# Kernel optimization log

Measured on AMD Instinct MI355X. Metric: run time of the kernel, lower is better.

The kernel has to match this reference:

```python
import jax, jax.numpy as jnp
import numpy as np

NUM_NODES = 1_000_000
MEM_DIM = 100
TIME_DIM = 100
EDGE_DIM = 172
HIDDEN = 128  # TGN_DECODER_HIDDEN
E = 500_000
IN_DIM = MEM_DIM * 2 + TIME_DIM + EDGE_DIM  # 472


def setup_inputs() -> dict:
    key = jax.random.key(0)
    ks = jax.random.split(key, 12)
    src = jax.random.randint(ks[0], (E,), 0, NUM_NODES)
    dst = jax.random.randint(ks[1], (E,), 0, NUM_NODES)
    t = jax.random.uniform(ks[2], (E,), dtype=jnp.float32) * 1000.0
    edge_attr = jax.random.normal(ks[3], (E, EDGE_DIM), dtype=jnp.float32)
    memory = jax.random.normal(ks[4], (NUM_NODES, MEM_DIM), dtype=jnp.float32)
    last_update = jax.random.uniform(ks[5], (NUM_NODES,), dtype=jnp.float32) * 500.0
    # TimeEncoder: cos(Linear(1, time_dim))
    time_w = jax.random.normal(ks[6], (TIME_DIM,), dtype=jnp.float32) / jnp.sqrt(1.0)
    time_b = jax.random.normal(ks[7], (TIME_DIM,), dtype=jnp.float32)
    # growth head: Linear(IN_DIM, HIDDEN) -> ReLU -> Linear(HIDDEN, 1)
    w1 = jax.random.normal(ks[8], (IN_DIM, HIDDEN), dtype=jnp.float32) / jnp.sqrt(IN_DIM)
    b1 = jnp.zeros((HIDDEN,), dtype=jnp.float32)
    w2 = jax.random.normal(ks[9], (HIDDEN, 1), dtype=jnp.float32) / jnp.sqrt(HIDDEN)
    b2 = jnp.zeros((1,), dtype=jnp.float32)
    return {"src": src, "dst": dst, "t": t, "edge_attr": edge_attr,
            "memory": memory, "last_update": last_update,
            "time_w": time_w, "time_b": time_b,
            "w1": w1, "b1": b1, "w2": w2, "b2": b2}


def reference(src, dst, t, edge_attr, memory, last_update, time_w, time_b, w1, b1, w2, b2):
    # Gather per-node memory rows (irregular indexing)
    src_mem = memory[src]                     # [E, MEM_DIM]
    dst_mem = memory[dst]                     # [E, MEM_DIM]
    delta_t = t - last_update[src]            # [E]
    # TimeEncoder: cos(delta_t * w + b)
    dt_enc = jnp.cos(delta_t[:, None] * time_w[None, :] + time_b[None, :])  # [E, TIME_DIM]
    out = jnp.concatenate([src_mem, dst_mem, dt_enc, edge_attr], axis=1)   # [E, IN_DIM]
    h = jax.nn.relu(out @ w1 + b1)            # [E, HIDDEN]
    growth_score = h @ w2 + b2                # [E, 1]
    return growth_score
```

## Files before the change

kernel.cpp:

```cpp
#include <hip/hip_runtime.h>
#include <hip/hip_bf16.h>
#include <math.h>

#define MEM_DIM  100
#define TIME_DIM 100
#define EDGE_DIM 172
#define HIDDEN   128
#define IN_DIM   472
#define K_PAD    480
#define NCHUNK   15
#define BM       256
#define THREADS  1024
#define W1_ELEMS (NCHUNK * 8 * 64 * 8)
#define W1_BYTES (W1_ELEMS * 2)

typedef __attribute__((ext_vector_type(8))) short bf16x8;
typedef __attribute__((ext_vector_type(4))) float floatx4;

typedef const __attribute__((address_space(1))) unsigned int* gp_t;
typedef __attribute__((address_space(3))) unsigned int* lp_t;

__global__ void prep_w1(const float* __restrict__ w1, __hip_bfloat16* __restrict__ w1p) {
    int idx = blockIdx.x * 256 + threadIdx.x;
    if (idx >= K_PAD * HIDDEN) return;
    int k = idx >> 7;
    int n = idx & 127;
    float v = (k < IN_DIM) ? w1[k * HIDDEN + n] : 0.0f;
    int c = k >> 5, kl = k & 31, quad = kl >> 3, j = kl & 7;
    int t = n >> 4, r = n & 15;
    int off = ((c * 8 + t) * 64 + quad * 16 + r) * 8 + j;
    w1p[off] = __float2bfloat16(v);
}

__global__ __launch_bounds__(THREADS, 4)
void tgn_mfma(const int* __restrict__ src, const int* __restrict__ dst,
              const float* __restrict__ t, const float* __restrict__ edge_attr,
              const float* __restrict__ memory, const float* __restrict__ last_update,
              const float* __restrict__ time_w, const float* __restrict__ time_b,
              const __hip_bfloat16* __restrict__ w1p, const float* __restrict__ b1,
              const float* __restrict__ w2, const float* __restrict__ b2,
              float* __restrict__ out, int E)
{
    extern __shared__ __hip_bfloat16 W1s[];
    __shared__ int   s_src[BM];
    __shared__ int   s_dst[BM];
    __shared__ float s_dt[BM];
    __shared__ float s_tw[TIME_DIM], s_tb[TIME_DIM];
    __shared__ float s_b1[HIDDEN], s_w2[HIDDEN];
    __shared__ float s_out[BM];

    const int tid  = threadIdx.x;
    const int e0   = blockIdx.x * BM;
    const int g    = tid >> 6;
    const int lane = tid & 63;
    const int quad = (tid >> 4) & 3;
    const int r    = tid & 15;

    #pragma unroll
    for (int i = 0; i < 8; ++i) {
        int off = i * (THREADS * 16) + tid * 16;
        if (off < W1_BYTES) {
            __builtin_amdgcn_global_load_lds(
                (gp_t)(const void*)((const char*)w1p + off),
                (lp_t)(void*)((char*)W1s + off), 16, 0, 0);
        }
    }
    if (tid < BM) {
        int e = e0 + tid; if (e >= E) e = E - 1;
        int s = src[e];
        s_src[tid] = s;
        s_dst[tid] = dst[e];
        s_dt[tid]  = t[e] - last_update[s];
    }
    if (tid < HIDDEN) { s_b1[tid] = b1[tid]; s_w2[tid] = w2[tid]; }
    if (tid < TIME_DIM) { s_tw[tid] = time_w[tid]; s_tb[tid] = time_b[tid]; }
    __syncthreads();

    const int m = g * 16 + r;
    const float* srcrow = memory + (long)s_src[m] * MEM_DIM;
    const float* dstrow = memory + (long)s_dst[m] * MEM_DIM;
    int em = e0 + m; if (em >= E) em = E - 1;
    const float* earow = edge_attr + (long)em * EDGE_DIM;
    const float dt = s_dt[m];

    floatx4 acc[8];
    #pragma unroll
    for (int i = 0; i < 8; ++i) acc[i] = (floatx4){0.f, 0.f, 0.f, 0.f};

    #pragma unroll
    for (int c = 0; c < NCHUNK; ++c) {
        const int kb = c * 32 + quad * 8;
        float v[8];
        if (kb + 7 < MEM_DIM) {
            float4 lo = *(const float4*)(srcrow + kb);
            float4 hi = *(const float4*)(srcrow + kb + 4);
            v[0]=lo.x; v[1]=lo.y; v[2]=lo.z; v[3]=lo.w;
            v[4]=hi.x; v[5]=hi.y; v[6]=hi.z; v[7]=hi.w;
        } else if (kb >= MEM_DIM && kb + 7 < 2 * MEM_DIM) {
            float4 lo = *(const float4*)(dstrow + kb - MEM_DIM);
            float4 hi = *(const float4*)(dstrow + kb - MEM_DIM + 4);
            v[0]=lo.x; v[1]=lo.y; v[2]=lo.z; v[3]=lo.w;
            v[4]=hi.x; v[5]=hi.y; v[6]=hi.z; v[7]=hi.w;
        } else if (kb >= 200 && kb + 7 < 300) {
            int c0 = kb - 200;
            #pragma unroll
            for (int j = 0; j < 8; ++j)
                v[j] = cosf(dt * s_tw[c0 + j] + s_tb[c0 + j]);
        } else if (kb >= 300 && kb + 7 < IN_DIM) {
            float4 lo = *(const float4*)(earow + kb - 300);
            float4 hi = *(const float4*)(earow + kb - 300 + 4);
            v[0]=lo.x; v[1]=lo.y; v[2]=lo.z; v[3]=lo.w;
            v[4]=hi.x; v[5]=hi.y; v[6]=hi.z; v[7]=hi.w;
        } else {
            #pragma unroll
            for (int j = 0; j < 8; ++j) {
                int k = kb + j;
                float x;
                if (k < MEM_DIM)          x = srcrow[k];
                else if (k < 2 * MEM_DIM) x = dstrow[k - MEM_DIM];
                else if (k < 300)         x = cosf(dt * s_tw[k - 200] + s_tb[k - 200]);
                else if (k < IN_DIM)      x = earow[k - 300];
                else                      x = 0.0f;
                v[j] = x;
            }
        }
        bf16x8 af;
        #pragma unroll
        for (int j = 0; j < 8; ++j)
            af[j] = (short)__bfloat16_as_ushort(__float2bfloat16(v[j]));

        #pragma unroll
        for (int tnum = 0; tnum < 8; ++tnum) {
            bf16x8 bfrag = ((bf16x8*)W1s)[(c * 8 + tnum) * 64 + lane];
            acc[tnum] = __builtin_amdgcn_mfma_f32_16x16x32_bf16(af, bfrag, acc[tnum], 0, 0, 0);
        }
    }

    float part[4] = {0.f, 0.f, 0.f, 0.f};
    #pragma unroll
    for (int tnum = 0; tnum < 8; ++tnum) {
        int n = tnum * 16 + r;
        float b1n = s_b1[n];
        float w2n = s_w2[n];
        #pragma unroll
        for (int reg = 0; reg < 4; ++reg) {
            float h = acc[tnum][reg] + b1n;
            h = h > 0.f ? h : 0.f;
            part[reg] += h * w2n;
        }
    }
    const float b2v = b2[0];
    #pragma unroll
    for (int reg = 0; reg < 4; ++reg) {
        float p = part[reg];
        p += __shfl_xor(p, 1, 64);
        p += __shfl_xor(p, 2, 64);
        p += __shfl_xor(p, 4, 64);
        p += __shfl_xor(p, 8, 64);
        if (r == 0) s_out[g * 16 + quad * 4 + reg] = p + b2v;
    }
    __syncthreads();
    if (tid < BM) {
        int e = e0 + tid;
        if (e < E) out[e] = s_out[tid];
    }
}

extern "C" void kernel_launch(void* const* d_in, const int* in_sizes, int n_in,
                              void* d_out, int out_size, void* d_ws, size_t ws_size,
                              hipStream_t stream) {
    const int*   src = (const int*)d_in[0];
    const int*   dst = (const int*)d_in[1];
    const float* t   = (const float*)d_in[2];
    const float* ea  = (const float*)d_in[3];
    const float* mem = (const float*)d_in[4];
    const float* lu  = (const float*)d_in[5];
    const float* tw  = (const float*)d_in[6];
    const float* tb  = (const float*)d_in[7];
    const float* w1  = (const float*)d_in[8];
    const float* b1  = (const float*)d_in[9];
    const float* w2  = (const float*)d_in[10];
    const float* b2  = (const float*)d_in[11];
    float* out = (float*)d_out;
    const int E = in_sizes[0];

    __hip_bfloat16* w1p = (__hip_bfloat16*)d_ws;

    static bool attr_set = false;
    if (!attr_set) {
        (void)hipFuncSetAttribute(reinterpret_cast<const void*>(tgn_mfma),
                                  hipFuncAttributeMaxDynamicSharedMemorySize,
                                  W1_BYTES);
        attr_set = true;
    }

    prep_w1<<<(K_PAD * HIDDEN + 255) / 256, 256, 0, stream>>>(w1, w1p);

    int grid = (E + BM - 1) / BM;
    tgn_mfma<<<grid, THREADS, W1_BYTES, stream>>>(src, dst, t, ea, mem, lu, tw, tb,
                                                  w1p, b1, w2, b2, out, E);
}
```

Measured before the change: 795.4 us.

## Pad each input segment to 128-wide K blocks and hoist all gather loads

Repacks W1 so each of the four input segments (src mem, dst mem, time enc, edge attr) starts at a 32-aligned chunk boundary, padding K from 480 to 576. Every per-lane load then becomes an aligned float4 with no per-element branching. All memory and edge-attr loads are issued early and the time-encoding MFMAs run first, so gather latency overlaps with compute. The cost is three extra MFMA chunks of zero padding, more LDS for W1 (fewer co-resident blocks possible) and higher register pressure from the hoisted loads.

New measurement: 792.2 us. Within noise of the previous version (-0.4%).

```diff
diff --git a/kernel.cpp b/kernel.cpp
--- a/kernel.cpp
+++ b/kernel.cpp
@@ -7,8 +7,8 @@
 #define EDGE_DIM 172
 #define HIDDEN   128
 #define IN_DIM   472
-#define K_PAD    480
-#define NCHUNK   15
+#define K_PAD    576
+#define NCHUNK   18
 #define BM       256
 #define THREADS  1024
 #define W1_ELEMS (NCHUNK * 8 * 64 * 8)
@@ -20,13 +20,20 @@
 typedef const __attribute__((address_space(1))) unsigned int* gp_t;
 typedef __attribute__((address_space(3))) unsigned int* lp_t;
 
+#define LD4(p) (*(const float4*)(p))
+
 __global__ void prep_w1(const float* __restrict__ w1, __hip_bfloat16* __restrict__ w1p) {
     int idx = blockIdx.x * 256 + threadIdx.x;
     if (idx >= K_PAD * HIDDEN) return;
-    int k = idx >> 7;
-    int n = idx & 127;
-    float v = (k < IN_DIM) ? w1[k * HIDDEN + n] : 0.0f;
-    int c = k >> 5, kl = k & 31, quad = kl >> 3, j = kl & 7;
+    int kp = idx >> 7;
+    int n  = idx & 127;
+    int k; bool valid;
+    if (kp < 128)      { k = kp;              valid = kp < 100; }
+    else if (kp < 256) { k = 100 + kp - 128;  valid = (kp - 128) < 100; }
+    else if (kp < 384) { k = 200 + kp - 256;  valid = (kp - 256) < 100; }
+    else               { k = 300 + kp - 384;  valid = (kp - 384) < 172; }
+    float v = valid ? w1[k * HIDDEN + n] : 0.0f;
+    int c = kp >> 5, kl = kp & 31, quad = kl >> 3, j = kl & 7;
     int t = n >> 4, r = n & 15;
     int off = ((c * 8 + t) * 64 + quad * 16 + r) * 8 + j;
     w1p[off] = __float2bfloat16(v);
@@ -57,13 +64,11 @@
     const int r    = tid & 15;
 
     #pragma unroll
-    for (int i = 0; i < 8; ++i) {
+    for (int i = 0; i < 9; ++i) {
         int off = i * (THREADS * 16) + tid * 16;
-        if (off < W1_BYTES) {
-            __builtin_amdgcn_global_load_lds(
-                (gp_t)(const void*)((const char*)w1p + off),
-                (lp_t)(void*)((char*)W1s + off), 16, 0, 0);
-        }
+        __builtin_amdgcn_global_load_lds(
+            (gp_t)(const void*)((const char*)w1p + off),
+            (lp_t)(void*)((char*)W1s + off), 16, 0, 0);
     }
     if (tid < BM) {
         int e = e0 + tid; if (e >= E) e = E - 1;
@@ -82,58 +87,126 @@
     int em = e0 + m; if (em >= E) em = E - 1;
     const float* earow = edge_attr + (long)em * EDGE_DIM;
     const float dt = s_dt[m];
+    const int qo = quad * 8;
 
     floatx4 acc[8];
     #pragma unroll
     for (int i = 0; i < 8; ++i) acc[i] = (floatx4){0.f, 0.f, 0.f, 0.f};
 
-    #pragma unroll
-    for (int c = 0; c < NCHUNK; ++c) {
-        const int kb = c * 32 + quad * 8;
-        float v[8];
-        if (kb + 7 < MEM_DIM) {
-            float4 lo = *(const float4*)(srcrow + kb);
-            float4 hi = *(const float4*)(srcrow + kb + 4);
-            v[0]=lo.x; v[1]=lo.y; v[2]=lo.z; v[3]=lo.w;
-            v[4]=hi.x; v[5]=hi.y; v[6]=hi.z; v[7]=hi.w;
-        } else if (kb >= MEM_DIM && kb + 7 < 2 * MEM_DIM) {
-            float4 lo = *(const float4*)(dstrow + kb - MEM_DIM);
-            float4 hi = *(const float4*)(dstrow + kb - MEM_DIM + 4);
-            v[0]=lo.x; v[1]=lo.y; v[2]=lo.z; v[3]=lo.w;
-            v[4]=hi.x; v[5]=hi.y; v[6]=hi.z; v[7]=hi.w;
-        } else if (kb >= 200 && kb + 7 < 300) {
-            int c0 = kb - 200;
-            #pragma unroll
-            for (int j = 0; j < 8; ++j)
-                v[j] = cosf(dt * s_tw[c0 + j] + s_tb[c0 + j]);
-        } else if (kb >= 300 && kb + 7 < IN_DIM) {
-            float4 lo = *(const float4*)(earow + kb - 300);
-            float4 hi = *(const float4*)(earow + kb - 300 + 4);
-            v[0]=lo.x; v[1]=lo.y; v[2]=lo.z; v[3]=lo.w;
-            v[4]=hi.x; v[5]=hi.y; v[6]=hi.z; v[7]=hi.w;
-        } else {
-            #pragma unroll
-            for (int j = 0; j < 8; ++j) {
-                int k = kb + j;
-                float x;
-                if (k < MEM_DIM)          x = srcrow[k];
-                else if (k < 2 * MEM_DIM) x = dstrow[k - MEM_DIM];
-                else if (k < 300)         x = cosf(dt * s_tw[k - 200] + s_tb[k - 200]);
-                else if (k < IN_DIM)      x = earow[k - 300];
-                else                      x = 0.0f;
-                v[j] = x;
-            }
-        }
+    auto do_chunk = [&](int c, const float* v) {
         bf16x8 af;
         #pragma unroll
         for (int j = 0; j < 8; ++j)
             af[j] = (short)__bfloat16_as_ushort(__float2bfloat16(v[j]));
-
         #pragma unroll
         for (int tnum = 0; tnum < 8; ++tnum) {
             bf16x8 bfrag = ((bf16x8*)W1s)[(c * 8 + tnum) * 64 + lane];
             acc[tnum] = __builtin_amdgcn_mfma_f32_16x16x32_bf16(af, bfrag, acc[tnum], 0, 0, 0);
         }
+    };
+
+    float4 s0a = LD4(srcrow + qo);       float4 s0b = LD4(srcrow + qo + 4);
+    float4 s1a = LD4(srcrow + 32 + qo);  float4 s1b = LD4(srcrow + 36 + qo);
+    float4 s2a = LD4(srcrow + 64 + qo);  float4 s2b = LD4(srcrow + 68 + qo);
+    float4 s3  = LD4(srcrow + 96);
+    float4 d0a = LD4(dstrow + qo);       float4 d0b = LD4(dstrow + qo + 4);
+    float4 d1a = LD4(dstrow + 32 + qo);  float4 d1b = LD4(dstrow + 36 + qo);
+    float4 d2a = LD4(dstrow + 64 + qo);  float4 d2b = LD4(dstrow + 68 + qo);
+    float4 d3  = LD4(dstrow + 96);
+
+    #pragma unroll
+    for (int c = 8; c < 11; ++c) {
+        int i0 = (c - 8) * 32 + qo;
+        float v[8];
+        #pragma unroll
+        for (int j = 0; j < 8; ++j)
+            v[j] = cosf(dt * s_tw[i0 + j] + s_tb[i0 + j]);
+        do_chunk(c, v);
+    }
+    {
+        bool p0 = (quad == 0);
+        float v[8];
+        #pragma unroll
+        for (int j = 0; j < 4; ++j) {
+            float cv = cosf(dt * s_tw[96 + j] + s_tb[96 + j]);
+            v[j] = p0 ? cv : 0.f;
+        }
+        v[4] = v[5] = v[6] = v[7] = 0.f;
+        do_chunk(11, v);
+    }
+
+    {
+        float v[8] = {s0a.x,s0a.y,s0a.z,s0a.w, s0b.x,s0b.y,s0b.z,s0b.w};
+        do_chunk(0, v);
+    }
+    {
+        float v[8] = {s1a.x,s1a.y,s1a.z,s1a.w, s1b.x,s1b.y,s1b.z,s1b.w};
+        do_chunk(1, v);
+    }
+    {
+        float v[8] = {s2a.x,s2a.y,s2a.z,s2a.w, s2b.x,s2b.y,s2b.z,s2b.w};
+        do_chunk(2, v);
+    }
+    {
+        bool p0 = (quad == 0);
+        float v[8] = {p0?s3.x:0.f, p0?s3.y:0.f, p0?s3.z:0.f, p0?s3.w:0.f,
+                      0.f, 0.f, 0.f, 0.f};
+        do_chunk(3, v);
+    }
+
+    float4 e0a = LD4(earow + qo);        float4 e0b = LD4(earow + qo + 4);
+    float4 e1a = LD4(earow + 32 + qo);   float4 e1b = LD4(earow + 36 + qo);
+    float4 e2a = LD4(earow + 64 + qo);   float4 e2b = LD4(earow + 68 + qo);
+    float4 e3a = LD4(earow + 96 + qo);   float4 e3b = LD4(earow + 100 + qo);
+    float4 e4a = LD4(earow + 128 + qo);  float4 e4b = LD4(earow + 132 + qo);
+    float4 e5a = LD4(earow + ((quad <= 1) ? 160 + qo : 160));
+    float4 e5b = LD4(earow + ((quad == 0) ? 164 : 160));
+
+    {
+        float v[8] = {d0a.x,d0a.y,d0a.z,d0a.w, d0b.x,d0b.y,d0b.z,d0b.w};
+        do_chunk(4, v);
+    }
+    {
+        float v[8] = {d1a.x,d1a.y,d1a.z,d1a.w, d1b.x,d1b.y,d1b.z,d1b.w};
+        do_chunk(5, v);
+    }
+    {
+        float v[8] = {d2a.x,d2a.y,d2a.z,d2a.w, d2b.x,d2b.y,d2b.z,d2b.w};
+        do_chunk(6, v);
+    }
+    {
+        bool p0 = (quad == 0);
+        float v[8] = {p0?d3.x:0.f, p0?d3.y:0.f, p0?d3.z:0.f, p0?d3.w:0.f,
+                      0.f, 0.f, 0.f, 0.f};
+        do_chunk(7, v);
+    }
+
+    {
+        float v[8] = {e0a.x,e0a.y,e0a.z,e0a.w, e0b.x,e0b.y,e0b.z,e0b.w};
+        do_chunk(12, v);
+    }
+    {
+        float v[8] = {e1a.x,e1a.y,e1a.z,e1a.w, e1b.x,e1b.y,e1b.z,e1b.w};
+        do_chunk(13, v);
+    }
+    {
+        float v[8] = {e2a.x,e2a.y,e2a.z,e2a.w, e2b.x,e2b.y,e2b.z,e2b.w};
+        do_chunk(14, v);
+    }
+    {
+        float v[8] = {e3a.x,e3a.y,e3a.z,e3a.w, e3b.x,e3b.y,e3b.z,e3b.w};
+        do_chunk(15, v);
+    }
+    {
+        float v[8] = {e4a.x,e4a.y,e4a.z,e4a.w, e4b.x,e4b.y,e4b.z,e4b.w};
+        do_chunk(16, v);
+    }
+    {
+        bool pA = (quad <= 1);
+        bool pB = (quad == 0);
+        float v[8] = {pA?e5a.x:0.f, pA?e5a.y:0.f, pA?e5a.z:0.f, pA?e5a.w:0.f,
+                      pB?e5b.x:0.f, pB?e5b.y:0.f, pB?e5b.z:0.f, pB?e5b.w:0.f};
+        do_chunk(17, v);
     }
 
     float part[4] = {0.f, 0.f, 0.f, 0.f};
```
